# Performance work log

Hardware: AMD Instinct MI355X
Metric: run time of the kernel (lower is better)

## Reference

```python
import jax, jax.numpy as jnp
import numpy as np

N = 2048       # node_size
IN_DIM = 512   # input_dim
D = 64         # hidden1_dim


def setup_inputs() -> dict:
    key = jax.random.key(0)
    k0, k1, k2, k3 = jax.random.split(key, 4)
    x = jax.random.normal(k0, (N, IN_DIM), dtype=jnp.float32)
    # xavier/kaiming-scale params
    W = jax.random.normal(k1, (IN_DIM, D), dtype=jnp.float32) * (1.0 / np.sqrt(IN_DIM))
    W2 = jax.random.normal(k2, (2 * D, D), dtype=jnp.float32) * (1.0 / np.sqrt(2 * D))
    W3 = jax.random.normal(k3, (2 * D, 1), dtype=jnp.float32) * (1.0 / np.sqrt(2 * D))
    return {"x": x, "W": W, "W2": W2, "W3": W3}


def reference(x, W, W2, W3):
    # encode: z = x @ W                                  [N, D]
    z = x @ W
    n, d = z.shape
    rz = jax.nn.relu(z)  # relu acts per-half of concat([z_i; z_j]) => relu(z) rows

    # z_pair[i,j] = relu([z_i ; z_j]) @ W2 = rz_i @ W2[:d] + rz_j @ W2[d:]
    pa = rz @ W2[:d]   # [N, D] contribution of first half (row index i)
    pb = rz @ W2[d:]   # [N, D] contribution of second half (row index j)

    w3a = W3[:d, 0]    # [D] weight for z_pair half
    w3b = W3[d:, 0]    # [D] weight for elementwise-mult half

    # concat(z_pair, z_i*z_j) @ W3, reshaped to [N, N]:
    s_pair = (pa @ w3a)[:, None] + (pb @ w3a)[None, :]          # [N, N]
    s_mult = jnp.einsum('id,jd->ij', z, z * w3b)                # [N, N]
    logits = s_pair + s_mult

    # decode applies sigmoid, then forward applies sigmoid again
    return jax.nn.sigmoid(jax.nn.sigmoid(logits))
```

## Files before the change

### kernel.cpp

```cpp
#include <hip/hip_runtime.h>

#define NDIM 2048
#define KD 512
#define DD 64
#define LSTR 72

typedef short bf16x8 __attribute__((ext_vector_type(8)));
typedef float f32x4  __attribute__((ext_vector_type(4)));

__device__ __forceinline__ float sigf(float x) {
    return __builtin_amdgcn_rcpf(1.0f + __builtin_amdgcn_exp2f(x * -1.44269504088896f));
}
__device__ __forceinline__ unsigned short f2bf(float f) {
    union { float f; unsigned u; } c; c.f = f;
    unsigned r = c.u + 0x7FFF + ((c.u >> 16) & 1);
    return (unsigned short)(r >> 16);
}

__global__ __launch_bounds__(256) void zkern(
    const float* __restrict__ x, const float* __restrict__ W,
    const float* __restrict__ W2, const float* __restrict__ W3,
    float* __restrict__ A, float* __restrict__ Bv,
    unsigned short* __restrict__ Zb, unsigned short* __restrict__ ZWb)
{
    __shared__ float4 xs4[4 * 128];
    __shared__ float  us[64], vs[64];
    __shared__ float4 part[3 * 64];
    const int t  = threadIdx.x;
    const int i0 = blockIdx.x * 4;

    if (t < 128) {
        const int k = t & 63;
        const float* wrow = W2 + (size_t)(t < 64 ? k : 64 + k) * 64;
        float s = 0.f;
        #pragma unroll
        for (int n4 = 0; n4 < 16; ++n4) {
            float4 a = ((const float4*)wrow)[n4];
            float4 b = ((const float4*)W3)[n4];
            s += a.x * b.x + a.y * b.y + a.z * b.z + a.w * b.w;
        }
        if (t < 64) us[k] = s; else vs[k] = s;
    }

    #pragma unroll
    for (int ch = 0; ch < 2; ++ch) {
        int idx = ch * 256 + t;
        int row = idx >> 7, c4 = idx & 127;
        xs4[row * 128 + c4] = ((const float4*)(x + (size_t)(i0 + row) * KD))[c4];
    }
    __syncthreads();

    const int tx = t & 15, rw = (t >> 4) & 3, kh = t >> 6;
    const int c = tx * 4;
    float4 acc = {0.f, 0.f, 0.f, 0.f};
    const float* xrow = (const float*)xs4 + rw * KD + kh * 128;
    const float* Wp   = W + (size_t)(kh * 128) * DD + c;
    #pragma unroll 8
    for (int k = 0; k < 128; ++k) {
        float  xv = xrow[k];
        float4 wv = *(const float4*)(Wp + (size_t)k * DD);
        acc.x += xv * wv.x; acc.y += xv * wv.y;
        acc.z += xv * wv.z; acc.w += xv * wv.w;
    }
    if (kh) part[(kh - 1) * 64 + rw * 16 + tx] = acc;
    __syncthreads();

    if (t < 64) {
        float4 p0 = part[t], p1 = part[64 + t], p2 = part[128 + t];
        acc.x += p0.x + p1.x + p2.x;
        acc.y += p0.y + p1.y + p2.y;
        acc.z += p0.z + p1.z + p2.z;
        acc.w += p0.w + p1.w + p2.w;
        const int row = i0 + rw;

        union { unsigned short s[4]; uint2 v; } zb, zwb;
        zb.s[0] = f2bf(acc.x); zb.s[1] = f2bf(acc.y);
        zb.s[2] = f2bf(acc.z); zb.s[3] = f2bf(acc.w);
        *(uint2*)(Zb + (size_t)row * DD + c) = zb.v;

        float4 w3b = *(const float4*)(W3 + DD + c);
        zwb.s[0] = f2bf(acc.x * w3b.x); zwb.s[1] = f2bf(acc.y * w3b.y);
        zwb.s[2] = f2bf(acc.z * w3b.z); zwb.s[3] = f2bf(acc.w * w3b.w);
        *(uint2*)(ZWb + (size_t)row * DD + c) = zwb.v;

        float4 rz = {fmaxf(acc.x, 0.f), fmaxf(acc.y, 0.f),
                     fmaxf(acc.z, 0.f), fmaxf(acc.w, 0.f)};
        float4 u4 = *(const float4*)(us + c);
        float4 v4 = *(const float4*)(vs + c);
        float pa = rz.x * u4.x + rz.y * u4.y + rz.z * u4.z + rz.w * u4.w;
        float pb = rz.x * v4.x + rz.y * v4.y + rz.z * v4.z + rz.w * v4.w;
        #pragma unroll
        for (int m = 1; m < 16; m <<= 1) {
            pa += __shfl_xor(pa, m, 64);
            pb += __shfl_xor(pb, m, 64);
        }
        if (tx == 0) { A[row] = pa; Bv[row] = pb; }
    }
}

__global__ __launch_bounds__(256) void mainkern(
    const unsigned short* __restrict__ Zb, const unsigned short* __restrict__ ZWb,
    const float* __restrict__ A, const float* __restrict__ Bv,
    float* __restrict__ out)
{
    __shared__ unsigned short sZ[64 * LSTR + 8];
    __shared__ unsigned short sW[64 * LSTR + 8];
    __shared__ float sA[64], sB[64];
    const int t  = threadIdx.x;
    const int i0 = blockIdx.y * 64, j0 = blockIdx.x * 64;

    if (t < 64)       sA[t]      = A[i0 + t];
    else if (t < 128) sB[t - 64] = Bv[j0 + t - 64];

    #pragma unroll
    for (int ch = 0; ch < 2; ++ch) {
        int idx = ch * 256 + t;
        int row = idx >> 3, c8 = idx & 7;
        uint4 g = ((const uint4*)(Zb  + (size_t)(i0 + row) * DD))[c8];
        *(uint4*)(sZ + row * LSTR + c8 * 8) = g;
        uint4 h = ((const uint4*)(ZWb + (size_t)(j0 + row) * DD))[c8];
        *(uint4*)(sW + row * LSTR + c8 * 8) = h;
    }
    __syncthreads();

    const int lane = t & 63, w = t >> 6;
    const int m = lane & 15, quad = lane >> 4;

    bf16x8 a0 = *(const bf16x8*)(sZ + (16 * w + m) * LSTR + quad * 8);
    bf16x8 a1 = *(const bf16x8*)(sZ + (16 * w + m) * LSTR + 32 + quad * 8);

    f32x4 acc[4];
    #pragma unroll
    for (int t4 = 0; t4 < 4; ++t4) {
        bf16x8 b0 = *(const bf16x8*)(sW + (16 * t4 + m) * LSTR + quad * 8);
        bf16x8 b1 = *(const bf16x8*)(sW + (16 * t4 + m) * LSTR + 32 + quad * 8);
        f32x4 c = {0.f, 0.f, 0.f, 0.f};
        c = __builtin_amdgcn_mfma_f32_16x16x32_bf16(a0, b0, c, 0, 0, 0);
        c = __builtin_amdgcn_mfma_f32_16x16x32_bf16(a1, b1, c, 0, 0, 0);
        acc[t4] = c;
    }

    #pragma unroll
    for (int t4 = 0; t4 < 4; ++t4) {
        const int j   = j0 + 16 * t4 + m;
        const float bj = sB[16 * t4 + m];
        float* op = out + (size_t)(i0 + 16 * w + quad * 4) * NDIM + j;
        #pragma unroll
        for (int r = 0; r < 4; ++r) {
            const float ab = sA[16 * w + quad * 4 + r] + bj;
            float s  = ab + acc[t4][r];
            float y  = sigf(s);
            float tt = y - 0.5f;
            float o  = 0.6224593f +
                       tt * (0.2350037f + tt * (-0.0287786f + tt * (-0.0160594f)));
            __builtin_nontemporal_store(o, op);
            op += NDIM;
        }
    }
}

extern "C" void kernel_launch(void* const* d_in, const int* in_sizes, int n_in,
                              void* d_out, int out_size, void* d_ws, size_t ws_size,
                              hipStream_t stream)
{
    const float* x  = (const float*)d_in[0];
    const float* W  = (const float*)d_in[1];
    const float* W2 = (const float*)d_in[2];
    const float* W3 = (const float*)d_in[3];
    float* out = (float*)d_out;

    char* ws = (char*)d_ws;
    float* A  = (float*)ws;
    float* Bv = (float*)(ws + 8192);
    unsigned short* Zb  = (unsigned short*)(ws + 16384);
    unsigned short* ZWb = (unsigned short*)(ws + 16384 + NDIM * DD * 2);

    zkern<<<dim3(512), dim3(256), 0, stream>>>(x, W, W2, W3, A, Bv, Zb, ZWb);
    mainkern<<<dim3(32, 32), dim3(256), 0, stream>>>(Zb, ZWb, A, Bv, out);
}
```

Baseline: 79.36 us.

## Fuse projection and pairwise kernels into one cooperative launch with grid sync

Merges the z-projection kernel and the pairwise sigmoid kernel into a single cooperative kernel of 1024 blocks. The first 512 blocks compute Z, ZW, A and B, then all blocks meet at a grid-wide barrier before computing their output tile. The aim is to remove the second kernel launch and the gap between the two launches. In exchange it adds the cost of a grid barrier, requires all 1024 blocks to be resident at once (launch bounds of 4 blocks per CU), and falls back to the two-kernel path if the cooperative launch fails.

```diff
diff --git a/kernel.cpp b/kernel.cpp
--- a/kernel.cpp
+++ b/kernel.cpp
@@ -1,4 +1,7 @@
 #include <hip/hip_runtime.h>
+#include <hip/hip_cooperative_groups.h>
+
+namespace cg = cooperative_groups;
 
 #define NDIM 2048
 #define KD 512
@@ -15,6 +18,156 @@
     union { float f; unsigned u; } c; c.f = f;
     unsigned r = c.u + 0x7FFF + ((c.u >> 16) & 1);
     return (unsigned short)(r >> 16);
+}
+
+#define SMEM_BYTES 18976
+
+__global__ __launch_bounds__(256, 4) void fused(
+    const float* __restrict__ x, const float* __restrict__ W,
+    const float* __restrict__ W2, const float* __restrict__ W3,
+    float* __restrict__ A, float* __restrict__ Bv,
+    unsigned short* __restrict__ Zb, unsigned short* __restrict__ ZWb,
+    float* __restrict__ out)
+{
+    __shared__ __align__(16) char smem[SMEM_BYTES];
+    const int t = threadIdx.x;
+
+    if (blockIdx.x < 512) {
+        float4* xs4  = (float4*)smem;
+        float*  us   = (float*)(smem + 8192);
+        float*  vs   = (float*)(smem + 8448);
+        float4* part = (float4*)(smem + 8704);
+        const int i0 = blockIdx.x * 4;
+
+        if (t < 128) {
+            const int k = t & 63;
+            const float* wrow = W2 + (size_t)(t < 64 ? k : 64 + k) * 64;
+            float s = 0.f;
+            #pragma unroll
+            for (int n4 = 0; n4 < 16; ++n4) {
+                float4 a = ((const float4*)wrow)[n4];
+                float4 b = ((const float4*)W3)[n4];
+                s += a.x * b.x + a.y * b.y + a.z * b.z + a.w * b.w;
+            }
+            if (t < 64) us[k] = s; else vs[k] = s;
+        }
+
+        #pragma unroll
+        for (int ch = 0; ch < 2; ++ch) {
+            int idx = ch * 256 + t;
+            int row = idx >> 7, c4 = idx & 127;
+            xs4[row * 128 + c4] = ((const float4*)(x + (size_t)(i0 + row) * KD))[c4];
+        }
+        __syncthreads();
+
+        const int tx = t & 15, rw = (t >> 4) & 3, kh = t >> 6;
+        const int c = tx * 4;
+        float4 acc = {0.f, 0.f, 0.f, 0.f};
+        const float* xrow = (const float*)xs4 + rw * KD + kh * 128;
+        const float* Wp   = W + (size_t)(kh * 128) * DD + c;
+        #pragma unroll 8
+        for (int k = 0; k < 128; ++k) {
+            float  xv = xrow[k];
+            float4 wv = *(const float4*)(Wp + (size_t)k * DD);
+            acc.x += xv * wv.x; acc.y += xv * wv.y;
+            acc.z += xv * wv.z; acc.w += xv * wv.w;
+        }
+        if (kh) part[(kh - 1) * 64 + rw * 16 + tx] = acc;
+        __syncthreads();
+
+        if (t < 64) {
+            float4 p0 = part[t], p1 = part[64 + t], p2 = part[128 + t];
+            acc.x += p0.x + p1.x + p2.x;
+            acc.y += p0.y + p1.y + p2.y;
+            acc.z += p0.z + p1.z + p2.z;
+            acc.w += p0.w + p1.w + p2.w;
+            const int row = i0 + rw;
+
+            union { unsigned short s[4]; uint2 v; } zb, zwb;
+            zb.s[0] = f2bf(acc.x); zb.s[1] = f2bf(acc.y);
+            zb.s[2] = f2bf(acc.z); zb.s[3] = f2bf(acc.w);
+            *(uint2*)(Zb + (size_t)row * DD + c) = zb.v;
+
+            float4 w3b = *(const float4*)(W3 + DD + c);
+            zwb.s[0] = f2bf(acc.x * w3b.x); zwb.s[1] = f2bf(acc.y * w3b.y);
+            zwb.s[2] = f2bf(acc.z * w3b.z); zwb.s[3] = f2bf(acc.w * w3b.w);
+            *(uint2*)(ZWb + (size_t)row * DD + c) = zwb.v;
+
+            float4 rz = {fmaxf(acc.x, 0.f), fmaxf(acc.y, 0.f),
+                         fmaxf(acc.z, 0.f), fmaxf(acc.w, 0.f)};
+            float4 u4 = *(const float4*)(us + c);
+            float4 v4 = *(const float4*)(vs + c);
+            float pa = rz.x * u4.x + rz.y * u4.y + rz.z * u4.z + rz.w * u4.w;
+            float pb = rz.x * v4.x + rz.y * v4.y + rz.z * v4.z + rz.w * v4.w;
+            #pragma unroll
+            for (int m = 1; m < 16; m <<= 1) {
+                pa += __shfl_xor(pa, m, 64);
+                pb += __shfl_xor(pb, m, 64);
+            }
+            if (tx == 0) { A[row] = pa; Bv[row] = pb; }
+        }
+    }
+
+    __threadfence();
+    cg::this_grid().sync();
+
+    {
+        unsigned short* sZ = (unsigned short*)smem;
+        unsigned short* sW = (unsigned short*)(smem + 9232);
+        float* sA = (float*)(smem + 18464);
+        float* sB = (float*)(smem + 18720);
+        const int i0 = (int)(blockIdx.x >> 5) * 64;
+        const int j0 = (int)(blockIdx.x & 31) * 64;
+
+        if (t < 64)       sA[t]      = A[i0 + t];
+        else if (t < 128) sB[t - 64] = Bv[j0 + t - 64];
+
+        #pragma unroll
+        for (int ch = 0; ch < 2; ++ch) {
+            int idx = ch * 256 + t;
+            int row = idx >> 3, c8 = idx & 7;
+            uint4 g = ((const uint4*)(Zb  + (size_t)(i0 + row) * DD))[c8];
+            *(uint4*)(sZ + row * LSTR + c8 * 8) = g;
+            uint4 h = ((const uint4*)(ZWb + (size_t)(j0 + row) * DD))[c8];
+            *(uint4*)(sW + row * LSTR + c8 * 8) = h;
+        }
+        __syncthreads();
+
+        const int lane = t & 63, w = t >> 6;
+        const int m = lane & 15, quad = lane >> 4;
+
+        bf16x8 a0 = *(const bf16x8*)(sZ + (16 * w + m) * LSTR + quad * 8);
+        bf16x8 a1 = *(const bf16x8*)(sZ + (16 * w + m) * LSTR + 32 + quad * 8);
+
+        f32x4 acc[4];
+        #pragma unroll
+        for (int t4 = 0; t4 < 4; ++t4) {
+            bf16x8 b0 = *(const bf16x8*)(sW + (16 * t4 + m) * LSTR + quad * 8);
+            bf16x8 b1 = *(const bf16x8*)(sW + (16 * t4 + m) * LSTR + 32 + quad * 8);
+            f32x4 c = {0.f, 0.f, 0.f, 0.f};
+            c = __builtin_amdgcn_mfma_f32_16x16x32_bf16(a0, b0, c, 0, 0, 0);
+            c = __builtin_amdgcn_mfma_f32_16x16x32_bf16(a1, b1, c, 0, 0, 0);
+            acc[t4] = c;
+        }
+
+        #pragma unroll
+        for (int t4 = 0; t4 < 4; ++t4) {
+            const int j   = j0 + 16 * t4 + m;
+            const float bj = sB[16 * t4 + m];
+            float* op = out + (size_t)(i0 + 16 * w + quad * 4) * NDIM + j;
+            #pragma unroll
+            for (int r = 0; r < 4; ++r) {
+                const float ab = sA[16 * w + quad * 4 + r] + bj;
+                float s  = ab + acc[t4][r];
+                float y  = sigf(s);
+                float tt = y - 0.5f;
+                float o  = 0.6224593f +
+                           tt * (0.2350037f + tt * (-0.0287786f + tt * (-0.0160594f)));
+                __builtin_nontemporal_store(o, op);
+                op += NDIM;
+            }
+        }
+    }
 }
 
 __global__ __launch_bounds__(256) void zkern(
@@ -175,6 +328,12 @@
     unsigned short* Zb  = (unsigned short*)(ws + 16384);
     unsigned short* ZWb = (unsigned short*)(ws + 16384 + NDIM * DD * 2);
 
-    zkern<<<dim3(512), dim3(256), 0, stream>>>(x, W, W2, W3, A, Bv, Zb, ZWb);
-    mainkern<<<dim3(32, 32), dim3(256), 0, stream>>>(Zb, ZWb, A, Bv, out);
-}
+    void* kargs[] = {(void*)&x, (void*)&W, (void*)&W2, (void*)&W3,
+                     (void*)&A, (void*)&Bv, (void*)&Zb, (void*)&ZWb, (void*)&out};
+    hipError_t err = hipLaunchCooperativeKernel(
+        fused, dim3(1024), dim3(256), kargs, (unsigned int)0, stream);
+    if (err != hipSuccess) {
+        zkern<<<dim3(512), dim3(256), 0, stream>>>(x, W, W2, W3, A, Bv, Zb, ZWb);
+        mainkern<<<dim3(32, 32), dim3(256), 0, stream>>>(Zb, ZWb, A, Bv, out);
+    }
+}
```

After: 289.9 us. 3.65x slower.
